# Optimization experiments

Measured on AMD Instinct MI355X. Metric: run time of the kernel, lower is better.

## Reference

```python
import jax, jax.numpy as jnp
import numpy as np

NODES = 512
SCALE_S, SCALE_M, SCALE_L = 512, 1024, 2048
BATCH = 16
SEQ = SCALE_S + SCALE_M + SCALE_L
EPS = 1e-5


def setup_inputs() -> dict:
    key = jax.random.key(0)
    ks = jax.random.split(key, 10)
    sd = 1.0 / np.sqrt(NODES)
    inp = {
        "x": jax.random.normal(ks[0], (BATCH, SEQ, NODES), dtype=jnp.float32),
        "gamma": jnp.ones((NODES,), jnp.float32),
        "beta": jnp.zeros((NODES,), jnp.float32),
        "Wqkv_s": jax.random.normal(ks[1], (NODES, 3 * NODES), jnp.float32) * sd,
        "bqkv_s": jnp.zeros((3 * NODES,), jnp.float32),
        "Wqkv_m": jax.random.normal(ks[2], (NODES, 3 * NODES), jnp.float32) * sd,
        "bqkv_m": jnp.zeros((3 * NODES,), jnp.float32),
        "Wqkv_l": jax.random.normal(ks[3], (NODES, 3 * NODES), jnp.float32) * sd,
        "bqkv_l": jnp.zeros((3 * NODES,), jnp.float32),
        "Wout": jax.random.normal(ks[4], (NODES, NODES), jnp.float32) * sd,
        "bout": jnp.zeros((NODES,), jnp.float32),
    }
    return inp


def _attn_block(x, W, b, scaling):
    # x: [B, L, N]; fused QKV projection then single-head attention
    qkv = jnp.einsum("bln,nm->blm", x, W) + b
    q, k, v = jnp.split(qkv, 3, axis=-1)
    scores = jnp.einsum("bqn,bkn->bqk", q, k) * scaling
    attn = jax.nn.softmax(scores, axis=-1)
    return jnp.einsum("bqk,bkn->bqn", attn, v)


def reference(x, gamma, beta, Wqkv_s, bqkv_s, Wqkv_m, bqkv_m, Wqkv_l, bqkv_l, Wout, bout):
    res = x
    mu = jnp.mean(x, axis=-1, keepdims=True)
    var = jnp.mean(jnp.square(x - mu), axis=-1, keepdims=True)
    h = (x - mu) * jax.lax.rsqrt(var + EPS) * gamma + beta

    scaling = NODES ** (-0.5)
    xs = h[:, :SCALE_S, :]
    xm = h[:, SCALE_S:SCALE_S + SCALE_M, :]
    xl = h[:, SCALE_S + SCALE_M:SCALE_S + SCALE_M + SCALE_L, :]

    out_s = _attn_block(xs, Wqkv_s, bqkv_s, scaling)
    out_m = _attn_block(xm, Wqkv_m, bqkv_m, scaling)
    out_l = _attn_block(xl, Wqkv_l, bqkv_l, scaling)

    out = jnp.concatenate([out_s, out_m, out_l], axis=1)
    out = jnp.einsum("bln,nm->blm", out, Wout) + bout
    return out + res
```

## Files before the change

kernel.cpp:

```cpp
#include <hip/hip_runtime.h>
#include <stdint.h>

typedef __bf16 bf16;
typedef __bf16 bf16x8 __attribute__((ext_vector_type(8)));
typedef __bf16 bf16x4 __attribute__((ext_vector_type(4)));
typedef float f32x4 __attribute__((ext_vector_type(4)));

#define MFMA16(a, b, c) __builtin_amdgcn_mfma_f32_16x16x32_bf16(a, b, c, 0, 0, 0)

typedef const __attribute__((address_space(1))) uint32_t* gas_t;
typedef __attribute__((address_space(3))) uint32_t* las_t;

__device__ __forceinline__ void gload16(const void* g, void* l) {
  __builtin_amdgcn_global_load_lds((gas_t)g, (las_t)l, 16, 0, 0);
}

__device__ __forceinline__ void stage_tile(const bf16* __restrict__ A, int lda,
                                           const bf16* __restrict__ Bt, int ldb,
                                           int m0, int n0, int k0, bf16* Ad,
                                           bf16* Bd, int w, int r8, int cs) {
#pragma unroll
  for (int i = 0; i < 4; ++i) {
    const int ii = (w << 2) + i;
    const int row = (ii << 3) + r8;
    gload16(A + (size_t)(m0 + row) * lda + k0 + (cs << 3), Ad + (ii << 9));
    gload16(Bt + (size_t)(n0 + row) * ldb + k0 + (cs << 3), Bd + (ii << 9));
  }
}

__device__ __forceinline__ void compute_tile(const bf16* As, const bf16* Bs,
                                             f32x4 (*acc)[4], int lane, int wm,
                                             int wn) {
#pragma unroll
  for (int kk = 0; kk < 2; ++kk) {
    bf16x8 af[4], bfr[4];
#pragma unroll
    for (int mi = 0; mi < 4; ++mi) {
      const int r = wm * 64 + mi * 16 + (lane & 15);
      const int ch = kk * 4 + (lane >> 4);
      af[mi] = *(const bf16x8*)((const char*)As + r * 128 + ((ch ^ (r & 7)) << 4));
    }
#pragma unroll
    for (int ni = 0; ni < 4; ++ni) {
      const int r = wn * 64 + ni * 16 + (lane & 15);
      const int ch = kk * 4 + (lane >> 4);
      bfr[ni] = *(const bf16x8*)((const char*)Bs + r * 128 + ((ch ^ (r & 7)) << 4));
    }
#pragma unroll
    for (int mi = 0; mi < 4; ++mi)
#pragma unroll
      for (int ni = 0; ni < 4; ++ni)
        acc[mi][ni] = MFMA16(af[mi], bfr[ni], acc[mi][ni]);
  }
}

__device__ __forceinline__ void gemm_core(const bf16* __restrict__ A, int lda,
                                          const bf16* __restrict__ Bt, int ldb,
                                          int nk, int m0, int n0,
                                          bf16 (*smem)[128 * 64],
                                          f32x4 (*acc)[4]) {
  const int t = threadIdx.x;
  const int lane = t & 63, w = t >> 6;
  const int wm = w >> 1, wn = w & 1;
  const int r8 = lane >> 3;
  const int cs = (lane & 7) ^ r8;

  stage_tile(A, lda, Bt, ldb, m0, n0, 0, smem[0], smem[2], w, r8, cs);
  __syncthreads();
  int cur = 0;
  for (int kt = 0; kt < nk; ++kt) {
    if (kt + 1 < nk)
      stage_tile(A, lda, Bt, ldb, m0, n0, (kt + 1) << 6, smem[cur ^ 1],
                 smem[2 + (cur ^ 1)], w, r8, cs);
    compute_tile(smem[cur], smem[2 + cur], acc, lane, wm, wn);
    __syncthreads();
    cur ^= 1;
  }
}

__device__ __forceinline__ void epi_put(float* lds, const f32x4* accmi,
                                        int lane, int wm, int wn) {
#pragma unroll
  for (int ni = 0; ni < 4; ++ni) {
    const int c = wn * 64 + ni * 16 + (lane & 15);
    const int lr0 = wm * 16 + ((lane >> 4) << 2);
#pragma unroll
    for (int r = 0; r < 4; ++r) {
      const int lr = lr0 + r;
      lds[(lr << 7) + ((((c >> 2) ^ (lr & 7)) << 2) | (c & 3))] = accmi[ni][r];
    }
  }
}

__device__ __forceinline__ void epi_get(const float* lds, int t, f32x4* v) {
  const int lr = t >> 3, ch0 = (t & 7) << 2;
#pragma unroll
  for (int j = 0; j < 4; ++j)
    v[j] = *(const f32x4*)(lds + (lr << 7) + (((ch0 + j) ^ (lr & 7)) << 2));
}

__global__ __launch_bounds__(256) void transpose_all(
    const float* __restrict__ Ws, const float* __restrict__ Wm,
    const float* __restrict__ Wl, const float* __restrict__ Wo,
    bf16* __restrict__ os, bf16* __restrict__ om, bf16* __restrict__ ol,
    bf16* __restrict__ oo) {
  __shared__ float tile[32][33];
  const int id = blockIdx.x;
  const float* in;
  bf16* outp;
  int N, bx;
  if (id < 768) { in = Ws; outp = os; N = 1536; bx = id; }
  else if (id < 1536) { in = Wm; outp = om; N = 1536; bx = id - 768; }
  else if (id < 2304) { in = Wl; outp = ol; N = 1536; bx = id - 1536; }
  else { in = Wo; outp = oo; N = 512; bx = id - 2304; }
  const int nbx = N >> 5;
  const int n0 = (bx % nbx) * 32, k0 = (bx / nbx) * 32;
  const int tx = threadIdx.x, ty = threadIdx.y;
#pragma unroll
  for (int i = 0; i < 4; ++i)
    tile[ty * 4 + i][tx] = in[(size_t)(k0 + ty * 4 + i) * N + n0 + tx];
  __syncthreads();
#pragma unroll
  for (int i = 0; i < 4; ++i)
    outp[(size_t)(n0 + ty * 4 + i) * 512 + k0 + tx] = (bf16)tile[tx][ty * 4 + i];
}

__global__ __launch_bounds__(256) void ln_kernel(const float* __restrict__ x,
                                                 const float* __restrict__ gamma,
                                                 const float* __restrict__ beta,
                                                 bf16* __restrict__ h) {
  const int t = threadIdx.x, lane = t & 63, w = t >> 6;
  const int row = blockIdx.x * 4 + w;
  const float* xr = x + (size_t)row * 512 + lane * 8;
  float4 v0 = *(const float4*)xr;
  float4 v1 = *(const float4*)(xr + 4);
  float s = v0.x + v0.y + v0.z + v0.w + v1.x + v1.y + v1.z + v1.w;
  float q = v0.x * v0.x + v0.y * v0.y + v0.z * v0.z + v0.w * v0.w +
            v1.x * v1.x + v1.y * v1.y + v1.z * v1.z + v1.w * v1.w;
#pragma unroll
  for (int off = 1; off < 64; off <<= 1) {
    s += __shfl_xor(s, off);
    q += __shfl_xor(q, off);
  }
  const float mean = s * (1.0f / 512.0f);
  const float var = q * (1.0f / 512.0f) - mean * mean;
  const float rs = rsqrtf(var + 1e-5f);
  float4 g0 = *(const float4*)(gamma + lane * 8);
  float4 g1 = *(const float4*)(gamma + lane * 8 + 4);
  float4 b0 = *(const float4*)(beta + lane * 8);
  float4 b1 = *(const float4*)(beta + lane * 8 + 4);
  const int bb = row / 3584;
  const int sp = row - bb * 3584;
  size_t drow;
  if (sp < 512)
    drow = (size_t)bb * 512 + sp;
  else if (sp < 1536)
    drow = 8192 + (size_t)bb * 1024 + (sp - 512);
  else
    drow = 24576 + (size_t)bb * 2048 + (sp - 1536);
  bf16x8 ov = {(bf16)((v0.x - mean) * rs * g0.x + b0.x),
               (bf16)((v0.y - mean) * rs * g0.y + b0.y),
               (bf16)((v0.z - mean) * rs * g0.z + b0.z),
               (bf16)((v0.w - mean) * rs * g0.w + b0.w),
               (bf16)((v1.x - mean) * rs * g1.x + b1.x),
               (bf16)((v1.y - mean) * rs * g1.y + b1.y),
               (bf16)((v1.z - mean) * rs * g1.z + b1.z),
               (bf16)((v1.w - mean) * rs * g1.w + b1.w)};
  *(bf16x8*)(h + drow * 512 + lane * 8) = ov;
}

__global__ __launch_bounds__(256) void qkv_gemm(const bf16* __restrict__ A,
                                                const bf16* __restrict__ Bt,
                                                const float* __restrict__ bias,
                                                bf16* __restrict__ qk,
                                                bf16* __restrict__ vt, int l2L,
                                                int nblk) {
  __shared__ bf16 smem[4][128 * 64];
  const int t = threadIdx.x, lane = t & 63, w = t >> 6;
  const int wm = w >> 1, wn = w & 1;
  const int lg = (blockIdx.x & 7) * (nblk >> 3) + (blockIdx.x >> 3);
  const int m0 = (lg / 12) << 7;
  const int n0 = (lg % 12) << 7;
  const int L = 1 << l2L;

  f32x4 acc[4][4];
#pragma unroll
  for (int i = 0; i < 4; ++i)
#pragma unroll
    for (int j = 0; j < 4; ++j) acc[i][j] = (f32x4)0.0f;

  gemm_core(A, 512, Bt, 512, 8, m0, n0, smem, acc);

  if (n0 < 1024) {
    float* et = (float*)smem;
#pragma unroll
    for (int mi = 0; mi < 4; ++mi) epi_put(et + (mi << 12), acc[mi], lane, wm, wn);
    __syncthreads();
    const int lr = t >> 3, c0l = (t & 7) << 4;
    const int gcol = n0 + c0l;
#pragma unroll
    for (int mi = 0; mi < 4; ++mi) {
      f32x4 v[4];
      epi_get(et + (mi << 12), t, v);
      const int grow = m0 + ((lr >> 4) << 6) + mi * 16 + (lr & 15);
      bf16x8 o0, o1;
#pragma unroll
      for (int j = 0; j < 4; ++j) {
        float4 bv = *(const float4*)(bias + gcol + j * 4);
#pragma unroll
        for (int k = 0; k < 4; ++k) {
          const bf16 val = (bf16)(v[j][k] + ((const float*)&bv)[k]);
          if (j < 2) o0[j * 4 + k] = val;
          else o1[(j - 2) * 4 + k] = val;
        }
      }
      bf16* dst = qk + (size_t)grow * 1024 + gcol;
      *(bf16x8*)dst = o0;
      *(bf16x8*)(dst + 8) = o1;
    }
  } else {
#pragma unroll
    for (int ni = 0; ni < 4; ++ni) {
      const int col = n0 + wn * 64 + ni * 16 + (lane & 15);
      const float bv = bias[col];
#pragma unroll
      for (int mi = 0; mi < 4; ++mi) {
        const int rb = m0 + wm * 64 + mi * 16 + ((lane >> 4) << 2);
        const int d = col - 1024;
        const int bi = rb >> l2L;
        const int kv = rb & (L - 1);
        bf16x4 pk = {(bf16)(acc[mi][ni][0] + bv), (bf16)(acc[mi][ni][1] + bv),
                     (bf16)(acc[mi][ni][2] + bv), (bf16)(acc[mi][ni][3] + bv)};
        *(bf16x4*)(vt + ((size_t)bi * 512 + d) * L + kv) = pk;
      }
    }
  }
}

__global__ __launch_bounds__(256) void sgemm(const bf16* __restrict__ qk,
                                             bf16* __restrict__ sbuf, int l2L,
                                             int b0, float scl2, int nblk,
                                             float* __restrict__ psum) {
  __shared__ bf16 smem[4][128 * 64];
  const int t = threadIdx.x, lane = t & 63, w = t >> 6;
  const int wm = w >> 1, wn = w & 1;
  const int L = 1 << l2L;
  const int l2nt = l2L - 7;
  const int lg = (blockIdx.x & 7) * (nblk >> 3) + (blockIdx.x >> 3);
  const int bi = lg >> (2 * l2nt);
  const int rem = lg & ((1 << (2 * l2nt)) - 1);
  const int m0 = (rem >> l2nt) << 7;
  const int n0 = (rem & ((1 << l2nt) - 1)) << 7;

  const bf16* Ab = qk + (size_t)(b0 + bi) * L * 1024;
  const bf16* Bb = Ab + 512;
  bf16* C = sbuf + (size_t)bi * L * L;

  f32x4 acc[4][4];
#pragma unroll
  for (int i = 0; i < 4; ++i)
#pragma unroll
    for (int j = 0; j < 4; ++j) acc[i][j] = (f32x4)0.0f;

  gemm_core(Ab, 1024, Bb, 1024, 8, m0, n0, smem, acc);

  float* et = (float*)smem;
#pragma unroll
  for (int mi = 0; mi < 4; ++mi) epi_put(et + (mi << 12), acc[mi], lane, wm, wn);
  __syncthreads();
  const int lr = t >> 3, c0l = (t & 7) << 4;
  const int tilej = n0 >> 7;
#pragma unroll
  for (int mi = 0; mi < 4; ++mi) {
    f32x4 v[4];
    epi_get(et + (mi << 12), t, v);
    const int grow = m0 + ((lr >> 4) << 6) + mi * 16 + (lr & 15);
    bf16x8 o0, o1;
    float ps = 0.0f;
#pragma unroll
    for (int j = 0; j < 4; ++j)
#pragma unroll
      for (int k = 0; k < 4; ++k) {
        const float e = exp2f(v[j][k] * scl2);
        const bf16 val = (bf16)e;
        ps += (float)val;
        if (j < 2) o0[j * 4 + k] = val;
        else o1[(j - 2) * 4 + k] = val;
      }
    bf16* dst = C + (size_t)grow * L + n0 + c0l;
    *(bf16x8*)dst = o0;
    *(bf16x8*)(dst + 8) = o1;
    ps += __shfl_xor(ps, 1);
    ps += __shfl_xor(ps, 2);
    ps += __shfl_xor(ps, 4);
    if ((t & 7) == 0) psum[((size_t)(bi * L + grow) << 4) + tilej] = ps;
  }
}

__global__ __launch_bounds__(256) void pvgemm(const bf16* __restrict__ sbuf,
                                              const bf16* __restrict__ vt,
                                              bf16* __restrict__ o, int l2L,
                                              int b0, int nblk,
                                              const float* __restrict__ psum) {
  __shared__ bf16 smem[4][128 * 64];
  const int t = threadIdx.x, lane = t & 63, w = t >> 6;
  const int wm = w >> 1, wn = w & 1;
  const int L = 1 << l2L;
  const int l2nt = l2L - 7;
  const int ntile = 1 << l2nt;
  const int lg = (blockIdx.x & 7) * (nblk >> 3) + (blockIdx.x >> 3);
  const int bi = lg >> (l2nt + 2);
  const int rem = lg & ((1 << (l2nt + 2)) - 1);
  const int m0 = (rem >> 2) << 7;
  const int n0 = (rem & 3) << 7;
  const int b = b0 + bi;

  const bf16* Ab = sbuf + (size_t)bi * L * L;
  const bf16* Bb = vt + (size_t)b * 512 * L;
  bf16* C = o + (size_t)b * L * 512;

  f32x4 acc[4][4];
#pragma unroll
  for (int i = 0; i < 4; ++i)
#pragma unroll
    for (int j = 0; j < 4; ++j) acc[i][j] = (f32x4)0.0f;

  gemm_core(Ab, L, Bb, L, L >> 6, m0, n0, smem, acc);

  float* et = (float*)smem;
#pragma unroll
  for (int mi = 0; mi < 4; ++mi) epi_put(et + (mi << 12), acc[mi], lane, wm, wn);
  __syncthreads();
  const int lr = t >> 3, c0l = (t & 7) << 4;
#pragma unroll
  for (int mi = 0; mi < 4; ++mi) {
    f32x4 v[4];
    epi_get(et + (mi << 12), t, v);
    const int grow = m0 + ((lr >> 4) << 6) + mi * 16 + (lr & 15);
    const float* pr = psum + ((size_t)(bi * L + grow) << 4);
    float rs = 0.0f;
    for (int j = 0; j < ntile; ++j) rs += pr[j];
    const float inv = 1.0f / rs;
    bf16x8 o0, o1;
#pragma unroll
    for (int j = 0; j < 4; ++j)
#pragma unroll
      for (int k = 0; k < 4; ++k) {
        const bf16 val = (bf16)(v[j][k] * inv);
        if (j < 2) o0[j * 4 + k] = val;
        else o1[(j - 2) * 4 + k] = val;
      }
    bf16* dst = C + (size_t)grow * 512 + n0 + c0l;
    *(bf16x8*)dst = o0;
    *(bf16x8*)(dst + 8) = o1;
  }
}

__device__ __forceinline__ int row2g(int row) {
  if (row < 8192) return ((row >> 9) * 3584) + (row & 511);
  if (row < 24576) {
    const int r = row - 8192;
    return ((r >> 10) * 3584) + 512 + (r & 1023);
  }
  const int r = row - 24576;
  return ((r >> 11) * 3584) + 1536 + (r & 2047);
}

__global__ __launch_bounds__(256) void out_gemm(const bf16* __restrict__ A,
                                                const bf16* __restrict__ Bt,
                                                const float* __restrict__ bias,
                                                const float* __restrict__ x,
                                                float* __restrict__ out) {
  __shared__ bf16 smem[4][128 * 64];
  const int t = threadIdx.x, lane = t & 63, w = t >> 6;
  const int wm = w >> 1, wn = w & 1;
  const int lg = (blockIdx.x & 7) * 224 + (blockIdx.x >> 3);
  const int m0 = (lg >> 2) << 7;
  const int n0 = (lg & 3) << 7;

  const int lr = t >> 3, c0l = (t & 7) << 4;
  const int gcol = n0 + c0l;
  int gidx[4];
  f32x4 xv[4][4];
  float4 bvv[4];
#pragma unroll
  for (int j = 0; j < 4; ++j) bvv[j] = *(const float4*)(bias + gcol + j * 4);
#pragma unroll
  for (int mi = 0; mi < 4; ++mi) {
    const int grow = m0 + ((lr >> 4) << 6) + mi * 16 + (lr & 15);
    gidx[mi] = row2g(grow);
#pragma unroll
    for (int j = 0; j < 4; ++j)
      xv[mi][j] = *(const f32x4*)(x + (size_t)gidx[mi] * 512 + gcol + j * 4);
  }

  f32x4 acc[4][4];
#pragma unroll
  for (int i = 0; i < 4; ++i)
#pragma unroll
    for (int j = 0; j < 4; ++j) acc[i][j] = (f32x4)0.0f;

  gemm_core(A, 512, Bt, 512, 8, m0, n0, smem, acc);

  float* et = (float*)smem;
#pragma unroll
  for (int mi = 0; mi < 4; ++mi) epi_put(et + (mi << 12), acc[mi], lane, wm, wn);
  __syncthreads();
#pragma unroll
  for (int mi = 0; mi < 4; ++mi) {
    f32x4 v[4];
    epi_get(et + (mi << 12), t, v);
    float* os = out + (size_t)gidx[mi] * 512 + gcol;
#pragma unroll
    for (int j = 0; j < 4; ++j) {
      float4 ov;
      ov.x = v[j][0] + bvv[j].x + xv[mi][j][0];
      ov.y = v[j][1] + bvv[j].y + xv[mi][j][1];
      ov.z = v[j][2] + bvv[j].z + xv[mi][j][2];
      ov.w = v[j][3] + bvv[j].w + xv[mi][j][3];
      *(float4*)(os + j * 4) = ov;
    }
  }
}

extern "C" void kernel_launch(void* const* d_in, const int* in_sizes, int n_in,
                              void* d_out, int out_size, void* d_ws,
                              size_t ws_size, hipStream_t stream) {
  const float* x = (const float*)d_in[0];
  const float* gamma = (const float*)d_in[1];
  const float* beta = (const float*)d_in[2];
  const float* Wq_s = (const float*)d_in[3];
  const float* bq_s = (const float*)d_in[4];
  const float* Wq_m = (const float*)d_in[5];
  const float* bq_m = (const float*)d_in[6];
  const float* Wq_l = (const float*)d_in[7];
  const float* bq_l = (const float*)d_in[8];
  const float* Wout = (const float*)d_in[9];
  const float* bout = (const float*)d_in[10];
  float* out = (float*)d_out;

  char* ws = (char*)d_ws;
  bf16* h = (bf16*)(ws);
  bf16* qk = (bf16*)(ws + 58720256ull);
  bf16* vt = (bf16*)(ws + 176160768ull);
  bf16* wt_s = (bf16*)(ws + 234881024ull);
  bf16* wt_m = (bf16*)(ws + 236453888ull);
  bf16* wt_l = (bf16*)(ws + 238026752ull);
  bf16* wt_o = (bf16*)(ws + 239599616ull);
  float* psum = (float*)(ws + 240124928ull);
  bf16* sbuf = (bf16*)d_out;

  transpose_all<<<2560, dim3(32, 8), 0, stream>>>(Wq_s, Wq_m, Wq_l, Wout, wt_s,
                                                  wt_m, wt_l, wt_o);

  ln_kernel<<<14336, 256, 0, stream>>>(x, gamma, beta, h);

  qkv_gemm<<<768, 256, 0, stream>>>(h, wt_s, bq_s, qk, vt, 9, 768);
  qkv_gemm<<<1536, 256, 0, stream>>>(h + 8192ull * 512, wt_m, bq_m,
                                     qk + 8192ull * 1024, vt + 4194304ull, 10,
                                     1536);
  qkv_gemm<<<3072, 256, 0, stream>>>(h + 24576ull * 512, wt_l, bq_l,
                                     qk + 24576ull * 1024, vt + 12582912ull,
                                     11, 3072);

  const float scale = 0.04419417382415922f;
  const float scl2 = scale * 1.44269504088896f;

  sgemm<<<256, 256, 0, stream>>>(qk, sbuf, 9, 0, scl2, 256, psum);
  pvgemm<<<256, 256, 0, stream>>>(sbuf, vt, h, 9, 0, 256, psum);

  sgemm<<<1024, 256, 0, stream>>>(qk + 8192ull * 1024, sbuf, 10, 0, scl2, 1024,
                                  psum);
  pvgemm<<<512, 256, 0, stream>>>(sbuf, vt + 4194304ull, h + 8192ull * 512, 10,
                                  0, 512, psum);

  for (int b0 = 0; b0 < 16; b0 += 8) {
    sgemm<<<2048, 256, 0, stream>>>(qk + 24576ull * 1024, sbuf, 11, b0, scl2,
                                    2048, psum);
    pvgemm<<<512, 256, 0, stream>>>(sbuf, vt + 12582912ull, h + 24576ull * 512,
                                    11, b0, 512, psum);
  }

  out_gemm<<<1792, 256, 0, stream>>>(h, wt_o, bout, x, out);
}
```

Baseline: 582.5 us.

## Single-buffer GEMM staging and halve LDS to raise occupancy

The GEMM core drops double-buffered LDS staging. It now loads one tile, syncs, computes and syncs again, so each kernel needs half the shared memory (32KB instead of 64KB). The epilogues stage the accumulators through LDS in two halves to fit the smaller buffer, and out_gemm loads the residual x inside the epilogue instead of holding it in registers across the GEMM. This should allow more resident blocks per CU, but it gives up the overlap of global loads with MFMA compute and adds barriers.

```diff
diff --git a/kernel.cpp b/kernel.cpp
--- a/kernel.cpp
+++ b/kernel.cpp
@@ -65,16 +65,11 @@
   const int r8 = lane >> 3;
   const int cs = (lane & 7) ^ r8;
 
-  stage_tile(A, lda, Bt, ldb, m0, n0, 0, smem[0], smem[2], w, r8, cs);
-  __syncthreads();
-  int cur = 0;
   for (int kt = 0; kt < nk; ++kt) {
-    if (kt + 1 < nk)
-      stage_tile(A, lda, Bt, ldb, m0, n0, (kt + 1) << 6, smem[cur ^ 1],
-                 smem[2 + (cur ^ 1)], w, r8, cs);
-    compute_tile(smem[cur], smem[2 + cur], acc, lane, wm, wn);
-    __syncthreads();
-    cur ^= 1;
+    stage_tile(A, lda, Bt, ldb, m0, n0, kt << 6, smem[0], smem[1], w, r8, cs);
+    __syncthreads();
+    compute_tile(smem[0], smem[1], acc, lane, wm, wn);
+    __syncthreads();
   }
 }
 
@@ -175,7 +170,7 @@
                                                 bf16* __restrict__ qk,
                                                 bf16* __restrict__ vt, int l2L,
                                                 int nblk) {
-  __shared__ bf16 smem[4][128 * 64];
+  __shared__ bf16 smem[2][128 * 64];
   const int t = threadIdx.x, lane = t & 63, w = t >> 6;
   const int wm = w >> 1, wn = w & 1;
   const int lg = (blockIdx.x & 7) * (nblk >> 3) + (blockIdx.x >> 3);
@@ -193,30 +188,35 @@
 
   if (n0 < 1024) {
     float* et = (float*)smem;
-#pragma unroll
-    for (int mi = 0; mi < 4; ++mi) epi_put(et + (mi << 12), acc[mi], lane, wm, wn);
-    __syncthreads();
     const int lr = t >> 3, c0l = (t & 7) << 4;
     const int gcol = n0 + c0l;
 #pragma unroll
-    for (int mi = 0; mi < 4; ++mi) {
-      f32x4 v[4];
-      epi_get(et + (mi << 12), t, v);
-      const int grow = m0 + ((lr >> 4) << 6) + mi * 16 + (lr & 15);
-      bf16x8 o0, o1;
-#pragma unroll
-      for (int j = 0; j < 4; ++j) {
-        float4 bv = *(const float4*)(bias + gcol + j * 4);
-#pragma unroll
-        for (int k = 0; k < 4; ++k) {
-          const bf16 val = (bf16)(v[j][k] + ((const float*)&bv)[k]);
-          if (j < 2) o0[j * 4 + k] = val;
-          else o1[(j - 2) * 4 + k] = val;
+    for (int half = 0; half < 2; ++half) {
+      __syncthreads();
+      epi_put(et, acc[half * 2 + 0], lane, wm, wn);
+      epi_put(et + 4096, acc[half * 2 + 1], lane, wm, wn);
+      __syncthreads();
+#pragma unroll
+      for (int s2 = 0; s2 < 2; ++s2) {
+        const int mi = half * 2 + s2;
+        f32x4 v[4];
+        epi_get(et + s2 * 4096, t, v);
+        const int grow = m0 + ((lr >> 4) << 6) + mi * 16 + (lr & 15);
+        bf16x8 o0, o1;
+#pragma unroll
+        for (int j = 0; j < 4; ++j) {
+          float4 bv = *(const float4*)(bias + gcol + j * 4);
+#pragma unroll
+          for (int k = 0; k < 4; ++k) {
+            const bf16 val = (bf16)(v[j][k] + ((const float*)&bv)[k]);
+            if (j < 2) o0[j * 4 + k] = val;
+            else o1[(j - 2) * 4 + k] = val;
+          }
         }
+        bf16* dst = qk + (size_t)grow * 1024 + gcol;
+        *(bf16x8*)dst = o0;
+        *(bf16x8*)(dst + 8) = o1;
       }
-      bf16* dst = qk + (size_t)grow * 1024 + gcol;
-      *(bf16x8*)dst = o0;
-      *(bf16x8*)(dst + 8) = o1;
     }
   } else {
 #pragma unroll
@@ -241,7 +241,7 @@
                                              bf16* __restrict__ sbuf, int l2L,
                                              int b0, float scl2, int nblk,
                                              float* __restrict__ psum) {
-  __shared__ bf16 smem[4][128 * 64];
+  __shared__ bf16 smem[2][128 * 64];
   const int t = threadIdx.x, lane = t & 63, w = t >> 6;
   const int wm = w >> 1, wn = w & 1;
   const int L = 1 << l2L;
@@ -265,35 +265,40 @@
   gemm_core(Ab, 1024, Bb, 1024, 8, m0, n0, smem, acc);
 
   float* et = (float*)smem;
-#pragma unroll
-  for (int mi = 0; mi < 4; ++mi) epi_put(et + (mi << 12), acc[mi], lane, wm, wn);
-  __syncthreads();
   const int lr = t >> 3, c0l = (t & 7) << 4;
   const int tilej = n0 >> 7;
 #pragma unroll
-  for (int mi = 0; mi < 4; ++mi) {
-    f32x4 v[4];
-    epi_get(et + (mi << 12), t, v);
-    const int grow = m0 + ((lr >> 4) << 6) + mi * 16 + (lr & 15);
-    bf16x8 o0, o1;
-    float ps = 0.0f;
-#pragma unroll
-    for (int j = 0; j < 4; ++j)
-#pragma unroll
-      for (int k = 0; k < 4; ++k) {
-        const float e = exp2f(v[j][k] * scl2);
-        const bf16 val = (bf16)e;
-        ps += (float)val;
-        if (j < 2) o0[j * 4 + k] = val;
-        else o1[(j - 2) * 4 + k] = val;
-      }
-    bf16* dst = C + (size_t)grow * L + n0 + c0l;
-    *(bf16x8*)dst = o0;
-    *(bf16x8*)(dst + 8) = o1;
-    ps += __shfl_xor(ps, 1);
-    ps += __shfl_xor(ps, 2);
-    ps += __shfl_xor(ps, 4);
-    if ((t & 7) == 0) psum[((size_t)(bi * L + grow) << 4) + tilej] = ps;
+  for (int half = 0; half < 2; ++half) {
+    __syncthreads();
+    epi_put(et, acc[half * 2 + 0], lane, wm, wn);
+    epi_put(et + 4096, acc[half * 2 + 1], lane, wm, wn);
+    __syncthreads();
+#pragma unroll
+    for (int s2 = 0; s2 < 2; ++s2) {
+      const int mi = half * 2 + s2;
+      f32x4 v[4];
+      epi_get(et + s2 * 4096, t, v);
+      const int grow = m0 + ((lr >> 4) << 6) + mi * 16 + (lr & 15);
+      bf16x8 o0, o1;
+      float ps = 0.0f;
+#pragma unroll
+      for (int j = 0; j < 4; ++j)
+#pragma unroll
+        for (int k = 0; k < 4; ++k) {
+          const float e = exp2f(v[j][k] * scl2);
+          const bf16 val = (bf16)e;
+          ps += (float)val;
+          if (j < 2) o0[j * 4 + k] = val;
+          else o1[(j - 2) * 4 + k] = val;
+        }
+      bf16* dst = C + (size_t)grow * L + n0 + c0l;
+      *(bf16x8*)dst = o0;
+      *(bf16x8*)(dst + 8) = o1;
+      ps += __shfl_xor(ps, 1);
+      ps += __shfl_xor(ps, 2);
+      ps += __shfl_xor(ps, 4);
+      if ((t & 7) == 0) psum[((size_t)(bi * L + grow) << 4) + tilej] = ps;
+    }
   }
 }
 
@@ -302,7 +307,7 @@
                                               bf16* __restrict__ o, int l2L,
                                               int b0, int nblk,
                                               const float* __restrict__ psum) {
-  __shared__ bf16 smem[4][128 * 64];
+  __shared__ bf16 smem[2][128 * 64];
   const int t = threadIdx.x, lane = t & 63, w = t >> 6;
   const int wm = w >> 1, wn = w & 1;
   const int L = 1 << l2L;
@@ -328,31 +333,36 @@
   gemm_core(Ab, L, Bb, L, L >> 6, m0, n0, smem, acc);
 
   float* et = (float*)smem;
-#pragma unroll
-  for (int mi = 0; mi < 4; ++mi) epi_put(et + (mi << 12), acc[mi], lane, wm, wn);
-  __syncthreads();
   const int lr = t >> 3, c0l = (t & 7) << 4;
 #pragma unroll
-  for (int mi = 0; mi < 4; ++mi) {
-    f32x4 v[4];
-    epi_get(et + (mi << 12), t, v);
-    const int grow = m0 + ((lr >> 4) << 6) + mi * 16 + (lr & 15);
-    const float* pr = psum + ((size_t)(bi * L + grow) << 4);
-    float rs = 0.0f;
-    for (int j = 0; j < ntile; ++j) rs += pr[j];
-    const float inv = 1.0f / rs;
-    bf16x8 o0, o1;
-#pragma unroll
-    for (int j = 0; j < 4; ++j)
-#pragma unroll
-      for (int k = 0; k < 4; ++k) {
-        const bf16 val = (bf16)(v[j][k] * inv);
-        if (j < 2) o0[j * 4 + k] = val;
-        else o1[(j - 2) * 4 + k] = val;
-      }
-    bf16* dst = C + (size_t)grow * 512 + n0 + c0l;
-    *(bf16x8*)dst = o0;
-    *(bf16x8*)(dst + 8) = o1;
+  for (int half = 0; half < 2; ++half) {
+    __syncthreads();
+    epi_put(et, acc[half * 2 + 0], lane, wm, wn);
+    epi_put(et + 4096, acc[half * 2 + 1], lane, wm, wn);
+    __syncthreads();
+#pragma unroll
+    for (int s2 = 0; s2 < 2; ++s2) {
+      const int mi = half * 2 + s2;
+      f32x4 v[4];
+      epi_get(et + s2 * 4096, t, v);
+      const int grow = m0 + ((lr >> 4) << 6) + mi * 16 + (lr & 15);
+      const float* pr = psum + ((size_t)(bi * L + grow) << 4);
+      float rs = 0.0f;
+      for (int j = 0; j < ntile; ++j) rs += pr[j];
+      const float inv = 1.0f / rs;
+      bf16x8 o0, o1;
+#pragma unroll
+      for (int j = 0; j < 4; ++j)
+#pragma unroll
+        for (int k = 0; k < 4; ++k) {
+          const bf16 val = (bf16)(v[j][k] * inv);
+          if (j < 2) o0[j * 4 + k] = val;
+          else o1[(j - 2) * 4 + k] = val;
+        }
+      bf16* dst = C + (size_t)grow * 512 + n0 + c0l;
+      *(bf16x8*)dst = o0;
+      *(bf16x8*)(dst + 8) = o1;
+    }
   }
 }
 
@@ -371,54 +381,52 @@
                                                 const float* __restrict__ bias,
                                                 const float* __restrict__ x,
                                                 float* __restrict__ out) {
-  __shared__ bf16 smem[4][128 * 64];
+  __shared__ bf16 smem[2][128 * 64];
   const int t = threadIdx.x, lane = t & 63, w = t >> 6;
   const int wm = w >> 1, wn = w & 1;
   const int lg = (blockIdx.x & 7) * 224 + (blockIdx.x >> 3);
   const int m0 = (lg >> 2) << 7;
   const int n0 = (lg & 3) << 7;
 
+  f32x4 acc[4][4];
+#pragma unroll
+  for (int i = 0; i < 4; ++i)
+#pragma unroll
+    for (int j = 0; j < 4; ++j) acc[i][j] = (f32x4)0.0f;
+
+  gemm_core(A, 512, Bt, 512, 8, m0, n0, smem, acc);
+
+  float* et = (float*)smem;
   const int lr = t >> 3, c0l = (t & 7) << 4;
   const int gcol = n0 + c0l;
-  int gidx[4];
-  f32x4 xv[4][4];
   float4 bvv[4];
 #pragma unroll
   for (int j = 0; j < 4; ++j) bvv[j] = *(const float4*)(bias + gcol + j * 4);
 #pragma unroll
-  for (int mi = 0; mi < 4; ++mi) {
-    const int grow = m0 + ((lr >> 4) << 6) + mi * 16 + (lr & 15);
-    gidx[mi] = row2g(grow);
-#pragma unroll
-    for (int j = 0; j < 4; ++j)
-      xv[mi][j] = *(const f32x4*)(x + (size_t)gidx[mi] * 512 + gcol + j * 4);
-  }
-
-  f32x4 acc[4][4];
-#pragma unroll
-  for (int i = 0; i < 4; ++i)
-#pragma unroll
-    for (int j = 0; j < 4; ++j) acc[i][j] = (f32x4)0.0f;
-
-  gemm_core(A, 512, Bt, 512, 8, m0, n0, smem, acc);
-
-  float* et = (float*)smem;
-#pragma unroll
-  for (int mi = 0; mi < 4; ++mi) epi_put(et + (mi << 12), acc[mi], lane, wm, wn);
-  __syncthreads();
-#pragma unroll
-  for (int mi = 0; mi < 4; ++mi) {
-    f32x4 v[4];
-    epi_get(et + (mi << 12), t, v);
-    float* os = out + (size_t)gidx[mi] * 512 + gcol;
-#pragma unroll
-    for (int j = 0; j < 4; ++j) {
-      float4 ov;
-      ov.x = v[j][0] + bvv[j].x + xv[mi][j][0];
-      ov.y = v[j][1] + bvv[j].y + xv[mi][j][1];
-      ov.z = v[j][2] + bvv[j].z + xv[mi][j][2];
-      ov.w = v[j][3] + bvv[j].w + xv[mi][j][3];
-      *(float4*)(os + j * 4) = ov;
+  for (int half = 0; half < 2; ++half) {
+    __syncthreads();
+    epi_put(et, acc[half * 2 + 0], lane, wm, wn);
+    epi_put(et + 4096, acc[half * 2 + 1], lane, wm, wn);
+    __syncthreads();
+#pragma unroll
+    for (int s2 = 0; s2 < 2; ++s2) {
+      const int mi = half * 2 + s2;
+      f32x4 v[4];
+      epi_get(et + s2 * 4096, t, v);
+      const int grow = m0 + ((lr >> 4) << 6) + mi * 16 + (lr & 15);
+      const int g = row2g(grow);
+      const float* xs = x + (size_t)g * 512 + gcol;
+      float* os = out + (size_t)g * 512 + gcol;
+#pragma unroll
+      for (int j = 0; j < 4; ++j) {
+        float4 xv = *(const float4*)(xs + j * 4);
+        float4 ov;
+        ov.x = v[j][0] + bvv[j].x + xv.x;
+        ov.y = v[j][1] + bvv[j].y + xv.y;
+        ov.z = v[j][2] + bvv[j].z + xv.z;
+        ov.w = v[j][3] + bvv[j].w + xv.w;
+        *(float4*)(os + j * 4) = ov;
+      }
     }
   }
 }
```

Result: slower. 652.8 us (+12.1%).

## Merge per-scale QKV, score and PV launches into grouped kernels

Applied to the files above, without the earlier changes.

Folds the three per-scale QKV GEMM launches into one grouped launch that picks scale by block index. The score and PV GEMMs for all three scales (first half of the long-scale batch) likewise run as single grouped launches. Score buffers and row sums are laid out side by side in the output buffer. This cuts launch count and the tail idle time between small kernels, but a single grid now mixes GEMMs with different K lengths, which can cause load imbalance.

```diff
diff --git a/kernel.cpp b/kernel.cpp
--- a/kernel.cpp
+++ b/kernel.cpp
@@ -169,18 +169,16 @@
   *(bf16x8*)(h + drow * 512 + lane * 8) = ov;
 }
 
-__global__ __launch_bounds__(256) void qkv_gemm(const bf16* __restrict__ A,
-                                                const bf16* __restrict__ Bt,
-                                                const float* __restrict__ bias,
-                                                bf16* __restrict__ qk,
-                                                bf16* __restrict__ vt, int l2L,
-                                                int nblk) {
-  __shared__ bf16 smem[4][128 * 64];
+__device__ __forceinline__ void qkv_body(const bf16* __restrict__ A,
+                                         const bf16* __restrict__ Bt,
+                                         const float* __restrict__ bias,
+                                         bf16* __restrict__ qk,
+                                         bf16* __restrict__ vt, int l2L,
+                                         int lgs, bf16 (*smem)[128 * 64]) {
   const int t = threadIdx.x, lane = t & 63, w = t >> 6;
   const int wm = w >> 1, wn = w & 1;
-  const int lg = (blockIdx.x & 7) * (nblk >> 3) + (blockIdx.x >> 3);
-  const int m0 = (lg / 12) << 7;
-  const int n0 = (lg % 12) << 7;
+  const int m0 = (lgs / 12) << 7;
+  const int n0 = (lgs % 12) << 7;
   const int L = 1 << l2L;
 
   f32x4 acc[4][4];
@@ -237,24 +235,42 @@
   }
 }
 
-__global__ __launch_bounds__(256) void sgemm(const bf16* __restrict__ qk,
-                                             bf16* __restrict__ sbuf, int l2L,
-                                             int b0, float scl2, int nblk,
-                                             float* __restrict__ psum) {
+__global__ __launch_bounds__(256) void qkv_all(
+    const bf16* __restrict__ h, const bf16* __restrict__ wt_s,
+    const bf16* __restrict__ wt_m, const bf16* __restrict__ wt_l,
+    const float* __restrict__ bq_s, const float* __restrict__ bq_m,
+    const float* __restrict__ bq_l, bf16* __restrict__ qk,
+    bf16* __restrict__ vt) {
   __shared__ bf16 smem[4][128 * 64];
+  const int lg = (blockIdx.x & 7) * (5376 >> 3) + (blockIdx.x >> 3);
+  if (lg < 768) {
+    qkv_body(h, wt_s, bq_s, qk, vt, 9, lg, smem);
+  } else if (lg < 2304) {
+    qkv_body(h + 8192ull * 512, wt_m, bq_m, qk + 8192ull * 1024,
+             vt + 4194304ull, 10, lg - 768, smem);
+  } else {
+    qkv_body(h + 24576ull * 512, wt_l, bq_l, qk + 24576ull * 1024,
+             vt + 12582912ull, 11, lg - 2304, smem);
+  }
+}
+
+__device__ __forceinline__ void sgemm_body(const bf16* __restrict__ qkp,
+                                           bf16* __restrict__ Cb, int l2L,
+                                           int b0, int lgs, float scl2,
+                                           float* __restrict__ psum, int psb,
+                                           bf16 (*smem)[128 * 64]) {
   const int t = threadIdx.x, lane = t & 63, w = t >> 6;
   const int wm = w >> 1, wn = w & 1;
   const int L = 1 << l2L;
   const int l2nt = l2L - 7;
-  const int lg = (blockIdx.x & 7) * (nblk >> 3) + (blockIdx.x >> 3);
-  const int bi = lg >> (2 * l2nt);
-  const int rem = lg & ((1 << (2 * l2nt)) - 1);
+  const int bi = lgs >> (2 * l2nt);
+  const int rem = lgs & ((1 << (2 * l2nt)) - 1);
   const int m0 = (rem >> l2nt) << 7;
   const int n0 = (rem & ((1 << l2nt) - 1)) << 7;
 
-  const bf16* Ab = qk + (size_t)(b0 + bi) * L * 1024;
+  const bf16* Ab = qkp + (size_t)(b0 + bi) * L * 1024;
   const bf16* Bb = Ab + 512;
-  bf16* C = sbuf + (size_t)bi * L * L;
+  bf16* C = Cb + (size_t)bi * L * L;
 
   f32x4 acc[4][4];
 #pragma unroll
@@ -293,31 +309,58 @@
     ps += __shfl_xor(ps, 1);
     ps += __shfl_xor(ps, 2);
     ps += __shfl_xor(ps, 4);
-    if ((t & 7) == 0) psum[((size_t)(bi * L + grow) << 4) + tilej] = ps;
-  }
-}
-
-__global__ __launch_bounds__(256) void pvgemm(const bf16* __restrict__ sbuf,
-                                              const bf16* __restrict__ vt,
-                                              bf16* __restrict__ o, int l2L,
-                                              int b0, int nblk,
-                                              const float* __restrict__ psum) {
+    if ((t & 7) == 0) psum[((size_t)(psb + bi * L + grow) << 4) + tilej] = ps;
+  }
+}
+
+__global__ __launch_bounds__(256) void sgemm_all(const bf16* __restrict__ qk,
+                                                 bf16* __restrict__ sbS,
+                                                 bf16* __restrict__ sbM,
+                                                 bf16* __restrict__ sbL,
+                                                 float scl2,
+                                                 float* __restrict__ psum) {
   __shared__ bf16 smem[4][128 * 64];
+  const int lg = (blockIdx.x & 7) * (3328 >> 3) + (blockIdx.x >> 3);
+  if (lg < 256) {
+    sgemm_body(qk, sbS, 9, 0, lg, scl2, psum, 0, smem);
+  } else if (lg < 1280) {
+    sgemm_body(qk + 8192ull * 1024, sbM, 10, 0, lg - 256, scl2, psum, 8192,
+               smem);
+  } else {
+    sgemm_body(qk + 24576ull * 1024, sbL, 11, 0, lg - 1280, scl2, psum, 24576,
+               smem);
+  }
+}
+
+__global__ __launch_bounds__(256) void sgemm_one(const bf16* __restrict__ qkp,
+                                                 bf16* __restrict__ Cb, int l2L,
+                                                 int b0, float scl2, int nblk,
+                                                 float* __restrict__ psum,
+                                                 int psb) {
+  __shared__ bf16 smem[4][128 * 64];
+  const int lg = (blockIdx.x & 7) * (nblk >> 3) + (blockIdx.x >> 3);
+  sgemm_body(qkp, Cb, l2L, b0, lg, scl2, psum, psb, smem);
+}
+
+__device__ __forceinline__ void pv_body(const bf16* __restrict__ sb,
+                                        const bf16* __restrict__ vtp,
+                                        bf16* __restrict__ op, int l2L, int b0,
+                                        int lgs, const float* __restrict__ psum,
+                                        int psb, bf16 (*smem)[128 * 64]) {
   const int t = threadIdx.x, lane = t & 63, w = t >> 6;
   const int wm = w >> 1, wn = w & 1;
   const int L = 1 << l2L;
   const int l2nt = l2L - 7;
   const int ntile = 1 << l2nt;
-  const int lg = (blockIdx.x & 7) * (nblk >> 3) + (blockIdx.x >> 3);
-  const int bi = lg >> (l2nt + 2);
-  const int rem = lg & ((1 << (l2nt + 2)) - 1);
+  const int bi = lgs >> (l2nt + 2);
+  const int rem = lgs & ((1 << (l2nt + 2)) - 1);
   const int m0 = (rem >> 2) << 7;
   const int n0 = (rem & 3) << 7;
   const int b = b0 + bi;
 
-  const bf16* Ab = sbuf + (size_t)bi * L * L;
-  const bf16* Bb = vt + (size_t)b * 512 * L;
-  bf16* C = o + (size_t)b * L * 512;
+  const bf16* Ab = sb + (size_t)bi * L * L;
+  const bf16* Bb = vtp + (size_t)b * 512 * L;
+  bf16* C = op + (size_t)b * L * 512;
 
   f32x4 acc[4][4];
 #pragma unroll
@@ -337,7 +380,7 @@
     f32x4 v[4];
     epi_get(et + (mi << 12), t, v);
     const int grow = m0 + ((lr >> 4) << 6) + mi * 16 + (lr & 15);
-    const float* pr = psum + ((size_t)(bi * L + grow) << 4);
+    const float* pr = psum + ((size_t)(psb + bi * L + grow) << 4);
     float rs = 0.0f;
     for (int j = 0; j < ntile; ++j) rs += pr[j];
     const float inv = 1.0f / rs;
@@ -354,6 +397,34 @@
     *(bf16x8*)dst = o0;
     *(bf16x8*)(dst + 8) = o1;
   }
+}
+
+__global__ __launch_bounds__(256) void pv_all(
+    const bf16* __restrict__ sbS, const bf16* __restrict__ sbM,
+    const bf16* __restrict__ sbL, const bf16* __restrict__ vt,
+    bf16* __restrict__ h, const float* __restrict__ psum) {
+  __shared__ bf16 smem[4][128 * 64];
+  const int lg = (blockIdx.x & 7) * (1280 >> 3) + (blockIdx.x >> 3);
+  if (lg < 256) {
+    pv_body(sbS, vt, h, 9, 0, lg, psum, 0, smem);
+  } else if (lg < 768) {
+    pv_body(sbM, vt + 4194304ull, h + 8192ull * 512, 10, 0, lg - 256, psum,
+            8192, smem);
+  } else {
+    pv_body(sbL, vt + 12582912ull, h + 24576ull * 512, 11, 0, lg - 768, psum,
+            24576, smem);
+  }
+}
+
+__global__ __launch_bounds__(256) void pv_one(const bf16* __restrict__ sb,
+                                              const bf16* __restrict__ vtp,
+                                              bf16* __restrict__ op, int l2L,
+                                              int b0, int nblk,
+                                              const float* __restrict__ psum,
+                                              int psb) {
+  __shared__ bf16 smem[4][128 * 64];
+  const int lg = (blockIdx.x & 7) * (nblk >> 3) + (blockIdx.x >> 3);
+  pv_body(sb, vtp, op, l2L, b0, lg, psum, psb, smem);
 }
 
 __device__ __forceinline__ int row2g(int row) {
@@ -447,39 +518,31 @@
   bf16* wt_m = (bf16*)(ws + 236453888ull);
   bf16* wt_l = (bf16*)(ws + 238026752ull);
   bf16* wt_o = (bf16*)(ws + 239599616ull);
-  float* psum = (float*)(ws + 240124928ull);
-  bf16* sbuf = (bf16*)d_out;
+
+  char* od = (char*)d_out;
+  bf16* sbS = (bf16*)od;
+  bf16* sbM = (bf16*)(od + 8388608ull);
+  bf16* sbL = (bf16*)(od + 41943040ull);
+  float* psum = (float*)(od + 109051904ull);
 
   transpose_all<<<2560, dim3(32, 8), 0, stream>>>(Wq_s, Wq_m, Wq_l, Wout, wt_s,
                                                   wt_m, wt_l, wt_o);
 
   ln_kernel<<<14336, 256, 0, stream>>>(x, gamma, beta, h);
 
-  qkv_gemm<<<768, 256, 0, stream>>>(h, wt_s, bq_s, qk, vt, 9, 768);
-  qkv_gemm<<<1536, 256, 0, stream>>>(h + 8192ull * 512, wt_m, bq_m,
-                                     qk + 8192ull * 1024, vt + 4194304ull, 10,
-                                     1536);
-  qkv_gemm<<<3072, 256, 0, stream>>>(h + 24576ull * 512, wt_l, bq_l,
-                                     qk + 24576ull * 1024, vt + 12582912ull,
-                                     11, 3072);
+  qkv_all<<<5376, 256, 0, stream>>>(h, wt_s, wt_m, wt_l, bq_s, bq_m, bq_l, qk,
+                                    vt);
 
   const float scale = 0.04419417382415922f;
   const float scl2 = scale * 1.44269504088896f;
 
-  sgemm<<<256, 256, 0, stream>>>(qk, sbuf, 9, 0, scl2, 256, psum);
-  pvgemm<<<256, 256, 0, stream>>>(sbuf, vt, h, 9, 0, 256, psum);
-
-  sgemm<<<1024, 256, 0, stream>>>(qk + 8192ull * 1024, sbuf, 10, 0, scl2, 1024,
-                                  psum);
-  pvgemm<<<512, 256, 0, stream>>>(sbuf, vt + 4194304ull, h + 8192ull * 512, 10,
-                                  0, 512, psum);
-
-  for (int b0 = 0; b0 < 16; b0 += 8) {
-    sgemm<<<2048, 256, 0, stream>>>(qk + 24576ull * 1024, sbuf, 11, b0, scl2,
-                                    2048, psum);
-    pvgemm<<<512, 256, 0, stream>>>(sbuf, vt + 12582912ull, h + 24576ull * 512,
-                                    11, b0, 512, psum);
-  }
+  sgemm_all<<<3328, 256, 0, stream>>>(qk, sbS, sbM, sbL, scl2, psum);
+  pv_all<<<1280, 256, 0, stream>>>(sbS, sbM, sbL, vt, h, psum);
+
+  sgemm_one<<<2048, 256, 0, stream>>>(qk + 24576ull * 1024, sbL, 11, 8, scl2,
+                                      2048, psum, 24576);
+  pv_one<<<512, 256, 0, stream>>>(sbL, vt + 12582912ull, h + 24576ull * 512,
+                                  11, 8, 512, psum, 24576);
 
   out_gemm<<<1792, 256, 0, stream>>>(h, wt_o, bout, x, out);
 }
```

New measurement: 594.3 us. +2.0%, slower.

## Fold output projection into V weights and fuse residual epilogue into PV GEMM

Applied to the files above, without the earlier changes.

Precomputes Wv·Wout per scale and folds the V bias through Wout, so the PV GEMM produces final outputs directly. Bias, residual add and softmax normalization move into the PV epilogue, which removes the separate output GEMM and its round trip of the attention output. The three QKV GEMMs are merged into one launch, and the large scale runs in four chunks of four batches. Scratch buffers for the folded weights are placed inside the output buffer, and the probability buffer reuses h. Folding the weights adds bf16 rounding of the product Wv·Wout.

```diff
diff --git a/kernel.cpp b/kernel.cpp
--- a/kernel.cpp
+++ b/kernel.cpp
@@ -123,6 +123,98 @@
 #pragma unroll
   for (int i = 0; i < 4; ++i)
     outp[(size_t)(n0 + ty * 4 + i) * 512 + k0 + tx] = (bf16)tile[tx][ty * 4 + i];
+}
+
+__global__ __launch_bounds__(256) void conv_v(const float* __restrict__ Ws,
+                                              const float* __restrict__ Wm,
+                                              const float* __restrict__ Wl,
+                                              bf16* __restrict__ Bs,
+                                              bf16* __restrict__ Bm,
+                                              bf16* __restrict__ Bl) {
+  int id = blockIdx.x;
+  const float* W;
+  bf16* B;
+  if (id < 256) { W = Ws; B = Bs; }
+  else if (id < 512) { W = Wm; B = Bm; id -= 256; }
+  else { W = Wl; B = Bl; id -= 512; }
+  const int idx = (id * 256 + threadIdx.x) * 4;
+  const int k = idx >> 9, j = idx & 511;
+  float4 v = *(const float4*)(W + (size_t)k * 1536 + 1024 + j);
+  bf16x4 o = {(bf16)v.x, (bf16)v.y, (bf16)v.z, (bf16)v.w};
+  *(bf16x4*)(B + idx) = o;
+}
+
+__global__ __launch_bounds__(256) void wprep(const bf16* __restrict__ wto,
+                                             const bf16* __restrict__ Bs,
+                                             const bf16* __restrict__ Bm,
+                                             const bf16* __restrict__ Bl,
+                                             bf16* __restrict__ ws_,
+                                             bf16* __restrict__ wm_,
+                                             bf16* __restrict__ wl_) {
+  __shared__ bf16 smem[4][128 * 64];
+  const int t = threadIdx.x, lane = t & 63, w = t >> 6;
+  const int wm = w >> 1, wn = w & 1;
+  const int id = blockIdx.x;
+  const int sc = id >> 4, rem = id & 15;
+  const bf16* Bv;
+  bf16* dst;
+  if (sc == 0) { Bv = Bs; dst = ws_; }
+  else if (sc == 1) { Bv = Bm; dst = wm_; }
+  else { Bv = Bl; dst = wl_; }
+  dst += 1024 * 512;
+  const int m0 = (rem >> 2) << 7, n0 = (rem & 3) << 7;
+
+  f32x4 acc[4][4];
+#pragma unroll
+  for (int i = 0; i < 4; ++i)
+#pragma unroll
+    for (int j = 0; j < 4; ++j) acc[i][j] = (f32x4)0.0f;
+
+  gemm_core(wto, 512, Bv, 512, 8, m0, n0, smem, acc);
+
+  float* et = (float*)smem;
+#pragma unroll
+  for (int mi = 0; mi < 4; ++mi) epi_put(et + (mi << 12), acc[mi], lane, wm, wn);
+  __syncthreads();
+  const int lr = t >> 3, c0l = (t & 7) << 4;
+#pragma unroll
+  for (int mi = 0; mi < 4; ++mi) {
+    f32x4 v[4];
+    epi_get(et + (mi << 12), t, v);
+    const int grow = m0 + ((lr >> 4) << 6) + mi * 16 + (lr & 15);
+    bf16x8 o0, o1;
+#pragma unroll
+    for (int j = 0; j < 4; ++j)
+#pragma unroll
+      for (int k = 0; k < 4; ++k) {
+        const bf16 val = (bf16)v[j][k];
+        if (j < 2) o0[j * 4 + k] = val;
+        else o1[(j - 2) * 4 + k] = val;
+      }
+    bf16* d = dst + (size_t)grow * 512 + n0 + c0l;
+    *(bf16x8*)d = o0;
+    *(bf16x8*)(d + 8) = o1;
+  }
+}
+
+__global__ __launch_bounds__(512) void bias_prep(const float* __restrict__ bs,
+                                                 const float* __restrict__ bm,
+                                                 const float* __restrict__ bl,
+                                                 const float* __restrict__ Wout,
+                                                 float* __restrict__ ps,
+                                                 float* __restrict__ pm,
+                                                 float* __restrict__ pl) {
+  const float* b;
+  float* p;
+  if (blockIdx.x == 0) { b = bs; p = ps; }
+  else if (blockIdx.x == 1) { b = bm; p = pm; }
+  else { b = bl; p = pl; }
+  const int t = threadIdx.x;
+  p[t] = b[t];
+  p[512 + t] = b[512 + t];
+  float acc = 0.0f;
+  for (int n = 0; n < 512; ++n) acc += b[1024 + n] * Wout[(size_t)n * 512 + t];
+  p[1024 + t] = acc;
 }
 
 __global__ __launch_bounds__(256) void ln_kernel(const float* __restrict__ x,
@@ -169,18 +261,16 @@
   *(bf16x8*)(h + drow * 512 + lane * 8) = ov;
 }
 
-__global__ __launch_bounds__(256) void qkv_gemm(const bf16* __restrict__ A,
-                                                const bf16* __restrict__ Bt,
-                                                const float* __restrict__ bias,
-                                                bf16* __restrict__ qk,
-                                                bf16* __restrict__ vt, int l2L,
-                                                int nblk) {
-  __shared__ bf16 smem[4][128 * 64];
+__device__ __forceinline__ void qkv_body(const bf16* __restrict__ A,
+                                         const bf16* __restrict__ Bt,
+                                         const float* __restrict__ bias,
+                                         bf16* __restrict__ qk,
+                                         bf16* __restrict__ vt, int l2L,
+                                         int lgs, bf16 (*smem)[128 * 64]) {
   const int t = threadIdx.x, lane = t & 63, w = t >> 6;
   const int wm = w >> 1, wn = w & 1;
-  const int lg = (blockIdx.x & 7) * (nblk >> 3) + (blockIdx.x >> 3);
-  const int m0 = (lg / 12) << 7;
-  const int n0 = (lg % 12) << 7;
+  const int m0 = (lgs / 12) << 7;
+  const int n0 = (lgs % 12) << 7;
   const int L = 1 << l2L;
 
   f32x4 acc[4][4];
@@ -237,24 +327,43 @@
   }
 }
 
-__global__ __launch_bounds__(256) void sgemm(const bf16* __restrict__ qk,
-                                             bf16* __restrict__ sbuf, int l2L,
-                                             int b0, float scl2, int nblk,
-                                             float* __restrict__ psum) {
+__global__ __launch_bounds__(256) void qkv_all(
+    const bf16* __restrict__ h, const bf16* __restrict__ wt_s,
+    const bf16* __restrict__ wt_m, const bf16* __restrict__ wt_l,
+    const float* __restrict__ pb_s, const float* __restrict__ pb_m,
+    const float* __restrict__ pb_l, bf16* __restrict__ qk,
+    bf16* __restrict__ vt) {
+  __shared__ bf16 smem[4][128 * 64];
+  const int lg = (blockIdx.x & 7) * (5376 >> 3) + (blockIdx.x >> 3);
+  if (lg < 768) {
+    qkv_body(h, wt_s, pb_s, qk, vt, 9, lg, smem);
+  } else if (lg < 2304) {
+    qkv_body(h + 8192ull * 512, wt_m, pb_m, qk + 8192ull * 1024,
+             vt + 4194304ull, 10, lg - 768, smem);
+  } else {
+    qkv_body(h + 24576ull * 512, wt_l, pb_l, qk + 24576ull * 1024,
+             vt + 12582912ull, 11, lg - 2304, smem);
+  }
+}
+
+__global__ __launch_bounds__(256) void sgemm_one(const bf16* __restrict__ qkp,
+                                                 bf16* __restrict__ Cb, int l2L,
+                                                 int b0, float scl2, int nblk,
+                                                 float* __restrict__ psum) {
   __shared__ bf16 smem[4][128 * 64];
   const int t = threadIdx.x, lane = t & 63, w = t >> 6;
   const int wm = w >> 1, wn = w & 1;
   const int L = 1 << l2L;
   const int l2nt = l2L - 7;
-  const int lg = (blockIdx.x & 7) * (nblk >> 3) + (blockIdx.x >> 3);
-  const int bi = lg >> (2 * l2nt);
-  const int rem = lg & ((1 << (2 * l2nt)) - 1);
+  const int lgs = (blockIdx.x & 7) * (nblk >> 3) + (blockIdx.x >> 3);
+  const int bi = lgs >> (2 * l2nt);
+  const int rem = lgs & ((1 << (2 * l2nt)) - 1);
   const int m0 = (rem >> l2nt) << 7;
   const int n0 = (rem & ((1 << l2nt) - 1)) << 7;
 
-  const bf16* Ab = qk + (size_t)(b0 + bi) * L * 1024;
+  const bf16* Ab = qkp + (size_t)(b0 + bi) * L * 1024;
   const bf16* Bb = Ab + 512;
-  bf16* C = sbuf + (size_t)bi * L * L;
+  bf16* C = Cb + (size_t)bi * L * L;
 
   f32x4 acc[4][4];
 #pragma unroll
@@ -297,10 +406,13 @@
   }
 }
 
-__global__ __launch_bounds__(256) void pvgemm(const bf16* __restrict__ sbuf,
-                                              const bf16* __restrict__ vt,
-                                              bf16* __restrict__ o, int l2L,
-                                              int b0, int nblk,
+__global__ __launch_bounds__(256) void pv_one(const bf16* __restrict__ sb,
+                                              const bf16* __restrict__ vtp,
+                                              float* __restrict__ out,
+                                              const float* __restrict__ x,
+                                              const float* __restrict__ bout,
+                                              int l2L, int b0, int seqoff,
+                                              int nblk,
                                               const float* __restrict__ psum) {
   __shared__ bf16 smem[4][128 * 64];
   const int t = threadIdx.x, lane = t & 63, w = t >> 6;
@@ -308,16 +420,15 @@
   const int L = 1 << l2L;
   const int l2nt = l2L - 7;
   const int ntile = 1 << l2nt;
-  const int lg = (blockIdx.x & 7) * (nblk >> 3) + (blockIdx.x >> 3);
-  const int bi = lg >> (l2nt + 2);
-  const int rem = lg & ((1 << (l2nt + 2)) - 1);
+  const int lgs = (blockIdx.x & 7) * (nblk >> 3) + (blockIdx.x >> 3);
+  const int bi = lgs >> (l2nt + 2);
+  const int rem = lgs & ((1 << (l2nt + 2)) - 1);
   const int m0 = (rem >> 2) << 7;
   const int n0 = (rem & 3) << 7;
   const int b = b0 + bi;
 
-  const bf16* Ab = sbuf + (size_t)bi * L * L;
-  const bf16* Bb = vt + (size_t)b * 512 * L;
-  bf16* C = o + (size_t)b * L * 512;
+  const bf16* Ab = sb + (size_t)bi * L * L;
+  const bf16* Bb = vtp + (size_t)b * 512 * L;
 
   f32x4 acc[4][4];
 #pragma unroll
@@ -332,6 +443,10 @@
   for (int mi = 0; mi < 4; ++mi) epi_put(et + (mi << 12), acc[mi], lane, wm, wn);
   __syncthreads();
   const int lr = t >> 3, c0l = (t & 7) << 4;
+  const int gcol = n0 + c0l;
+  float4 bvv[4];
+#pragma unroll
+  for (int j = 0; j < 4; ++j) bvv[j] = *(const float4*)(bout + gcol + j * 4);
 #pragma unroll
   for (int mi = 0; mi < 4; ++mi) {
     f32x4 v[4];
@@ -341,83 +456,17 @@
     float rs = 0.0f;
     for (int j = 0; j < ntile; ++j) rs += pr[j];
     const float inv = 1.0f / rs;
-    bf16x8 o0, o1;
-#pragma unroll
-    for (int j = 0; j < 4; ++j)
-#pragma unroll
-      for (int k = 0; k < 4; ++k) {
-        const bf16 val = (bf16)(v[j][k] * inv);
-        if (j < 2) o0[j * 4 + k] = val;
-        else o1[(j - 2) * 4 + k] = val;
-      }
-    bf16* dst = C + (size_t)grow * 512 + n0 + c0l;
-    *(bf16x8*)dst = o0;
-    *(bf16x8*)(dst + 8) = o1;
-  }
-}
-
-__device__ __forceinline__ int row2g(int row) {
-  if (row < 8192) return ((row >> 9) * 3584) + (row & 511);
-  if (row < 24576) {
-    const int r = row - 8192;
-    return ((r >> 10) * 3584) + 512 + (r & 1023);
-  }
-  const int r = row - 24576;
-  return ((r >> 11) * 3584) + 1536 + (r & 2047);
-}
-
-__global__ __launch_bounds__(256) void out_gemm(const bf16* __restrict__ A,
-                                                const bf16* __restrict__ Bt,
-                                                const float* __restrict__ bias,
-                                                const float* __restrict__ x,
-                                                float* __restrict__ out) {
-  __shared__ bf16 smem[4][128 * 64];
-  const int t = threadIdx.x, lane = t & 63, w = t >> 6;
-  const int wm = w >> 1, wn = w & 1;
-  const int lg = (blockIdx.x & 7) * 224 + (blockIdx.x >> 3);
-  const int m0 = (lg >> 2) << 7;
-  const int n0 = (lg & 3) << 7;
-
-  const int lr = t >> 3, c0l = (t & 7) << 4;
-  const int gcol = n0 + c0l;
-  int gidx[4];
-  f32x4 xv[4][4];
-  float4 bvv[4];
-#pragma unroll
-  for (int j = 0; j < 4; ++j) bvv[j] = *(const float4*)(bias + gcol + j * 4);
-#pragma unroll
-  for (int mi = 0; mi < 4; ++mi) {
-    const int grow = m0 + ((lr >> 4) << 6) + mi * 16 + (lr & 15);
-    gidx[mi] = row2g(grow);
-#pragma unroll
-    for (int j = 0; j < 4; ++j)
-      xv[mi][j] = *(const f32x4*)(x + (size_t)gidx[mi] * 512 + gcol + j * 4);
-  }
-
-  f32x4 acc[4][4];
-#pragma unroll
-  for (int i = 0; i < 4; ++i)
-#pragma unroll
-    for (int j = 0; j < 4; ++j) acc[i][j] = (f32x4)0.0f;
-
-  gemm_core(A, 512, Bt, 512, 8, m0, n0, smem, acc);
-
-  float* et = (float*)smem;
-#pragma unroll
-  for (int mi = 0; mi < 4; ++mi) epi_put(et + (mi << 12), acc[mi], lane, wm, wn);
-  __syncthreads();
-#pragma unroll
-  for (int mi = 0; mi < 4; ++mi) {
-    f32x4 v[4];
-    epi_get(et + (mi << 12), t, v);
-    float* os = out + (size_t)gidx[mi] * 512 + gcol;
+    const size_t g = (size_t)b * 3584 + seqoff + grow;
+    const float* xs = x + g * 512 + gcol;
+    float* os = out + g * 512 + gcol;
 #pragma unroll
     for (int j = 0; j < 4; ++j) {
+      float4 xv = *(const float4*)(xs + j * 4);
       float4 ov;
-      ov.x = v[j][0] + bvv[j].x + xv[mi][j][0];
-      ov.y = v[j][1] + bvv[j].y + xv[mi][j][1];
-      ov.z = v[j][2] + bvv[j].z + xv[mi][j][2];
-      ov.w = v[j][3] + bvv[j].w + xv[mi][j][3];
+      ov.x = v[j][0] * inv + bvv[j].x + xv.x;
+      ov.y = v[j][1] * inv + bvv[j].y + xv.y;
+      ov.z = v[j][2] * inv + bvv[j].z + xv.z;
+      ov.w = v[j][3] * inv + bvv[j].w + xv.w;
       *(float4*)(os + j * 4) = ov;
     }
   }
@@ -447,39 +496,43 @@
   bf16* wt_m = (bf16*)(ws + 236453888ull);
   bf16* wt_l = (bf16*)(ws + 238026752ull);
   bf16* wt_o = (bf16*)(ws + 239599616ull);
-  float* psum = (float*)(ws + 240124928ull);
-  bf16* sbuf = (bf16*)d_out;
+  float* psum = (float*)(ws + 240123904ull);
+
+  char* od = (char*)d_out;
+  bf16* Bv_s = (bf16*)(od + 110000128ull);
+  bf16* Bv_m = Bv_s + 262144;
+  bf16* Bv_l = Bv_m + 262144;
+  float* pb_s = (float*)(od + 111573504ull);
+  float* pb_m = pb_s + 1536;
+  float* pb_l = pb_m + 1536;
 
   transpose_all<<<2560, dim3(32, 8), 0, stream>>>(Wq_s, Wq_m, Wq_l, Wout, wt_s,
                                                   wt_m, wt_l, wt_o);
+  conv_v<<<768, 256, 0, stream>>>(Wq_s, Wq_m, Wq_l, Bv_s, Bv_m, Bv_l);
+  wprep<<<48, 256, 0, stream>>>(wt_o, Bv_s, Bv_m, Bv_l, wt_s, wt_m, wt_l);
+  bias_prep<<<3, 512, 0, stream>>>(bq_s, bq_m, bq_l, Wout, pb_s, pb_m, pb_l);
 
   ln_kernel<<<14336, 256, 0, stream>>>(x, gamma, beta, h);
 
-  qkv_gemm<<<768, 256, 0, stream>>>(h, wt_s, bq_s, qk, vt, 9, 768);
-  qkv_gemm<<<1536, 256, 0, stream>>>(h + 8192ull * 512, wt_m, bq_m,
-                                     qk + 8192ull * 1024, vt + 4194304ull, 10,
-                                     1536);
-  qkv_gemm<<<3072, 256, 0, stream>>>(h + 24576ull * 512, wt_l, bq_l,
-                                     qk + 24576ull * 1024, vt + 12582912ull,
-                                     11, 3072);
+  qkv_all<<<5376, 256, 0, stream>>>(h, wt_s, wt_m, wt_l, pb_s, pb_m, pb_l, qk,
+                                    vt);
 
   const float scale = 0.04419417382415922f;
   const float scl2 = scale * 1.44269504088896f;
-
-  sgemm<<<256, 256, 0, stream>>>(qk, sbuf, 9, 0, scl2, 256, psum);
-  pvgemm<<<256, 256, 0, stream>>>(sbuf, vt, h, 9, 0, 256, psum);
-
-  sgemm<<<1024, 256, 0, stream>>>(qk + 8192ull * 1024, sbuf, 10, 0, scl2, 1024,
-                                  psum);
-  pvgemm<<<512, 256, 0, stream>>>(sbuf, vt + 4194304ull, h + 8192ull * 512, 10,
-                                  0, 512, psum);
-
-  for (int b0 = 0; b0 < 16; b0 += 8) {
-    sgemm<<<2048, 256, 0, stream>>>(qk + 24576ull * 1024, sbuf, 11, b0, scl2,
-                                    2048, psum);
-    pvgemm<<<512, 256, 0, stream>>>(sbuf, vt + 12582912ull, h + 24576ull * 512,
-                                    11, b0, 512, psum);
-  }
-
-  out_gemm<<<1792, 256, 0, stream>>>(h, wt_o, bout, x, out);
-}
+  bf16* P = h;
+
+  sgemm_one<<<256, 256, 0, stream>>>(qk, P, 9, 0, scl2, 256, psum);
+  pv_one<<<256, 256, 0, stream>>>(P, vt, out, x, bout, 9, 0, 0, 256, psum);
+
+  sgemm_one<<<1024, 256, 0, stream>>>(qk + 8192ull * 1024, P, 10, 0, scl2,
+                                      1024, psum);
+  pv_one<<<512, 256, 0, stream>>>(P, vt + 4194304ull, out, x, bout, 10, 0, 512,
+                                  512, psum);
+
+  for (int q = 0; q < 4; ++q) {
+    sgemm_one<<<1024, 256, 0, stream>>>(qk + 24576ull * 1024, P, 11, q * 4,
+                                        scl2, 1024, psum);
+    pv_one<<<256, 256, 0, stream>>>(P, vt + 12582912ull, out, x, bout, 11,
+                                    q * 4, 1536, 256, psum);
+  }
+}
```

Measured after the change: 639.1 us. 1.1x slower.
